# Performance work log

Measured on AMD Instinct MI355X. Metric: run time of the kernel, lower is better.

Reference implementation:

```python
import jax, jax.numpy as jnp
import numpy as np

D_MODEL = 192
D_STATE = 128
D_CONV = 4
EXPAND = 2
D_INNER = EXPAND * D_MODEL            # 384
D_HALF = D_INNER // 2                 # 192 (x and z channel count)
DT_RANK = -(-D_MODEL // 16)           # ceil(192/16) = 12
B, H, W = 8, 32, 32


def serpentine(x):
    # flip every odd row along width: x (b, c, h, w)
    return x.at[:, :, 1::2, :].set(jnp.flip(x[:, :, 1::2, :], axis=3))


def causal_dwconv_silu(x, w):
    # x: (b, d, l), w: (d, k). Left-pad -> causal depthwise conv, then silu.
    k = w.shape[1]
    L = x.shape[-1]
    xp = jnp.pad(x, ((0, 0), (0, 0), (k - 1, 0)))
    y = jnp.zeros_like(x)
    for i in range(k):  # k=4, tiny fixed loop
        y = y + w[:, i][None, :, None] * xp[:, :, i:i + L]
    return jax.nn.silu(y)


def selective_scan(u, delta, A, Bm, Cm, Dp):
    # u, delta: (b, d, l); Bm, Cm: (b, n, l); A: (d, n); Dp: (d,)
    b, d, L = u.shape
    n = A.shape[1]

    def step(h, xs):
        u_t, dt_t, B_t, C_t = xs  # (b,d), (b,d), (b,n), (b,n)
        dA = jnp.exp(dt_t[:, :, None] * A)                      # (b,d,n)
        h = dA * h + (dt_t * u_t)[:, :, None] * B_t[:, None, :]
        y = jnp.einsum('bdn,bn->bd', h, C_t)
        return h, y

    xs = (jnp.moveaxis(u, 2, 0), jnp.moveaxis(delta, 2, 0),
          jnp.moveaxis(Bm, 2, 0), jnp.moveaxis(Cm, 2, 0))
    h0 = jnp.zeros((b, d, n), u.dtype)
    _, ys = jax.lax.scan(step, h0, xs)                          # (l, b, d)
    return jnp.moveaxis(ys, 0, 2).reshape(b, d, L) + Dp[None, :, None] * u


def setup_inputs() -> dict:
    key = jax.random.key(0)
    ks = jax.random.split(key, 8)
    hidden_states = jax.random.normal(ks[0], (B, D_MODEL, H, W), jnp.float32)
    W_in = jax.random.normal(ks[1], (D_INNER, D_MODEL), jnp.float32) * 0.02
    conv_w_x = jax.random.normal(ks[2], (D_HALF, D_CONV), jnp.float32) * 0.2
    conv_w_z = jax.random.normal(ks[3], (D_HALF, D_CONV), jnp.float32) * 0.2
    W_xproj = jax.random.normal(ks[4], (DT_RANK + 2 * D_STATE, D_HALF), jnp.float32) * 0.02
    dt_std = DT_RANK ** (-0.5)
    W_dt = jax.random.uniform(ks[5], (D_HALF, DT_RANK), jnp.float32, -dt_std, dt_std)
    # inv-softplus init of dt bias, as in the module
    dt = jnp.exp(jax.random.uniform(ks[6], (D_HALF,), jnp.float32)
                 * (np.log(0.1) - np.log(0.001)) + np.log(0.001))
    dt = jnp.clip(dt, 1e-4, None)
    b_dt = dt + jnp.log(-jnp.expm1(-dt))
    A_log = jnp.log(jnp.broadcast_to(jnp.arange(1, D_STATE + 1, dtype=jnp.float32),
                                     (D_HALF, D_STATE)))
    D_param = jnp.ones((D_HALF,), jnp.float32)
    W_out = jax.random.normal(ks[7], (D_MODEL, D_INNER), jnp.float32) * 0.02
    return {"hidden_states": hidden_states, "W_in": W_in, "conv_w_x": conv_w_x,
            "conv_w_z": conv_w_z, "W_xproj": W_xproj, "W_dt": W_dt, "b_dt": b_dt,
            "A_log": A_log, "D_param": D_param, "W_out": W_out}


def reference(hidden_states, W_in, conv_w_x, conv_w_z, W_xproj, W_dt, b_dt,
              A_log, D_param, W_out):
    b, c, h, w = hidden_states.shape
    L = h * w
    hs = serpentine(hidden_states)
    hs = hs.reshape(b, c, L).transpose(0, 2, 1)                 # (b, l, c)
    xz = hs @ W_in.T                                            # (b, l, 2d)
    xz = xz.transpose(0, 2, 1)                                  # (b, 2d, l)
    x, z = xz[:, :D_HALF], xz[:, D_HALF:]
    A = -jnp.exp(A_log.astype(jnp.float32))                     # (d, n)
    x = causal_dwconv_silu(x, conv_w_x)
    z = causal_dwconv_silu(z, conv_w_z)
    x_dbl = x.transpose(0, 2, 1) @ W_xproj.T                    # (b, l, r+2n)
    dt = x_dbl[..., :DT_RANK]
    Bm = x_dbl[..., DT_RANK:DT_RANK + D_STATE].transpose(0, 2, 1)  # (b, n, l)
    Cm = x_dbl[..., DT_RANK + D_STATE:].transpose(0, 2, 1)         # (b, n, l)
    dt = (dt @ W_dt.T + b_dt).transpose(0, 2, 1)                # (b, d, l), bias once
    # module passes delta_bias=dt_proj.bias again with delta_softplus=True
    delta = jax.nn.softplus(dt + b_dt[None, :, None])           # bias twice, faithful
    y = selective_scan(x, delta, A, Bm, Cm, D_param.astype(jnp.float32))
    y = jnp.concatenate([y, z], axis=1)                         # (b, 2d, l)
    out = y.transpose(0, 2, 1) @ W_out.T                        # (b, l, c)
    out = out.transpose(0, 2, 1).reshape(b, c, h, w)
    return serpentine(out)
```

## Files before the change

### kernel.cpp

```cpp
#include <hip/hip_runtime.h>
#include <math.h>

#define NB  8
#define DM  192
#define DH  192
#define DI  384
#define DS  128
#define DTR 12
#define XR  268
#define L   1024
#define NC  16
#define CL  64
#define NWX 320
#define LOG2E 1.44269504f

__device__ __forceinline__ void wave_lds_sync() {
  __builtin_amdgcn_wave_barrier();
  asm volatile("s_waitcnt lgkmcnt(0)" ::: "memory");
  __builtin_amdgcn_sched_barrier(0);
}

__global__ void k_wt_all(const float* __restrict__ Win,
                         const float* __restrict__ Wx,
                         const float* __restrict__ Wout,
                         float* __restrict__ wt_in,
                         float* __restrict__ wt_x,
                         float* __restrict__ wt_out) {
  const int j = blockIdx.x * 256 + threadIdx.x;
  const int k = blockIdx.y;
  const int z = blockIdx.z;
  if (z == 0) {
    if (k < 192 && j < 384) wt_in[(size_t)k * 384 + j] = Win[(size_t)j * 192 + k];
  } else if (z == 1) {
    if (k < 192 && j < NWX) wt_x[(size_t)k * NWX + j] = (j < XR) ? Wx[(size_t)j * 192 + k] : 0.f;
  } else {
    if (k < 384 && j < 192) wt_out[(size_t)k * 192 + j] = Wout[(size_t)j * 384 + k];
  }
}

template<int K, int N, int NW, int SERP_IN, int OMODE, int DODT>
__global__ __launch_bounds__(256) void k_gemm(const float* __restrict__ A,
                                              const float* __restrict__ Wt,
                                              float* __restrict__ Out,
                                              const float* __restrict__ Wdt,
                                              const float* __restrict__ bdt,
                                              float* __restrict__ dlt) {
  __shared__ __align__(16) float At2[48][64][4];
  __shared__ float xdl[DODT ? 64 * 13 : 1];
  const int lane = threadIdx.x & 63;
  const int wv   = threadIdx.x >> 6;
  const int l    = blockIdx.x * 64 + lane;
  const int n0   = __builtin_amdgcn_readfirstlane(blockIdx.y * 32 + wv * 8);
  const int b    = blockIdx.z;
  int lg = l;
  if (SERP_IN || OMODE == 2) {
    int h = l >> 5, w = l & 31;
    lg = h * 32 + ((h & 1) ? (31 - w) : w);
  }
  const float* Ab = A + (size_t)b * K * L + (SERP_IN ? lg : l);
  float acc[8];
#pragma unroll
  for (int i = 0; i < 8; ++i) acc[i] = 0.f;

  for (int k0 = 0; k0 < K; k0 += 192) {
    if (k0) __syncthreads();
#pragma unroll
    for (int i = 0; i < 48; ++i) {
      const int kr = wv * 48 + i;
      At2[kr >> 2][lane][kr & 3] = Ab[(size_t)(k0 + kr) * L];
    }
    __syncthreads();
#pragma unroll 8
    for (int kk4 = 0; kk4 < 48; ++kk4) {
      float4 a4 = *(const float4*)&At2[kk4][lane][0];
      float av[4] = {a4.x, a4.y, a4.z, a4.w};
#pragma unroll
      for (int j = 0; j < 4; ++j) {
        const float* wr = Wt + (size_t)(k0 + kk4 * 4 + j) * NW + n0;
        float a = av[j];
#pragma unroll
        for (int i = 0; i < 8; ++i) acc[i] = fmaf(wr[i], a, acc[i]);
      }
    }
  }

  if (OMODE == 0) {
    float* o = Out + ((size_t)b * N + n0) * L + l;
#pragma unroll
    for (int i = 0; i < 8; ++i) o[(size_t)i * L] = acc[i];
  } else if (OMODE == 1) {
    float* o = Out + ((size_t)b * L + l) * XR;
#pragma unroll
    for (int i = 0; i < 8; i += 4) {
      if (n0 + i + 4 <= XR)
        *(float4*)(o + n0 + i) = make_float4(acc[i], acc[i + 1], acc[i + 2], acc[i + 3]);
    }
  } else {
    float* o = Out + ((size_t)b * N + n0) * L + lg;
#pragma unroll
    for (int i = 0; i < 8; ++i) o[(size_t)i * L] = acc[i];
  }

  if constexpr (DODT) {
    if (blockIdx.y == 0) {
      if (wv == 0) {
#pragma unroll
        for (int i = 0; i < 8; ++i) xdl[lane * 13 + i] = acc[i];
      } else if (wv == 1) {
#pragma unroll
        for (int i = 0; i < 4; ++i) xdl[lane * 13 + 8 + i] = acc[i];
      }
      __syncthreads();
      float x[12];
#pragma unroll
      for (int r = 0; r < 12; ++r) x[r] = xdl[lane * 13 + r];
      const int dlo = wv * 48;
      for (int d = dlo; d < dlo + 48; ++d) {
        const float* wd = Wdt + d * DTR;
        float s = 2.f * bdt[d];
#pragma unroll
        for (int r = 0; r < DTR; ++r) s = fmaf(wd[r], x[r], s);
        float v = (s > 20.f) ? s : __logf(1.f + __expf(s));
        dlt[((size_t)b * DH + d) * L + l] = v;
      }
    }
  }
}

__global__ void k_conv_silu(const float* __restrict__ xz,
                            const float* __restrict__ cwx,
                            const float* __restrict__ cwz,
                            float* __restrict__ u,
                            float* __restrict__ ycat) {
  int idx = blockIdx.x * blockDim.x + threadIdx.x;
  const int per = NB * DH * (L / 4);
  int part = idx / per;
  int rem  = idx - part * per;
  int l4 = (rem & (L / 4 - 1)) * 4;
  int bd = rem >> 8;
  int d  = bd % DH;
  int b  = bd / DH;
  const float* cw = (part ? cwz : cwx) + d * 4;
  float w0 = cw[0], w1 = cw[1], w2 = cw[2], w3 = cw[3];
  const float* src = xz + ((size_t)b * DI + (part ? DH + d : d)) * L;
  float4 cur = *(const float4*)(src + l4);
  float pm3 = 0.f, pm2 = 0.f, pm1 = 0.f;
  if (l4 >= 4) {
    float4 p = *(const float4*)(src + l4 - 4);
    pm3 = p.y; pm2 = p.z; pm1 = p.w;
  }
  float s0 = fmaf(w3, cur.x, fmaf(w2, pm1,   fmaf(w1, pm2,   w0 * pm3)));
  float s1 = fmaf(w3, cur.y, fmaf(w2, cur.x, fmaf(w1, pm1,   w0 * pm2)));
  float s2 = fmaf(w3, cur.z, fmaf(w2, cur.y, fmaf(w1, cur.x, w0 * pm1)));
  float s3 = fmaf(w3, cur.w, fmaf(w2, cur.z, fmaf(w1, cur.y, w0 * cur.x)));
  float4 y;
  y.x = s0 / (1.f + __expf(-s0));
  y.y = s1 / (1.f + __expf(-s1));
  y.z = s2 / (1.f + __expf(-s2));
  y.w = s3 / (1.f + __expf(-s3));
  float* dst = part ? (ycat + ((size_t)b * DI + DH + d) * L + l4)
                    : (u + (size_t)bd * L + l4);
  *(float4*)dst = y;
}

__global__ void __launch_bounds__(256) k_scan1(const float* __restrict__ xdbl,
                                               const float* __restrict__ delta,
                                               const float* __restrict__ u,
                                               const float* __restrict__ Alog,
                                               float* __restrict__ hpart,
                                               float* __restrict__ apart) {
  __shared__ __align__(16) float dd[4][64][8];
  const int lane = threadIdx.x & 63;
  const int wv   = threadIdx.x >> 6;
  const int d0   = blockIdx.x * 8 + wv * 2;
  const int c = blockIdx.y, b = blockIdx.z;
  const int bd0 = b * DH + d0, bd1 = bd0 + 1;
  const float a00 = -__expf(Alog[(size_t)d0 * DS + 2 * lane]) * LOG2E;
  const float a10 = -__expf(Alog[(size_t)(d0 + 1) * DS + 2 * lane]) * LOG2E;
  const float* xrow  = xdbl + ((size_t)b * L + c * CL) * XR + DTR + 2 * lane;
  const float* drow0 = delta + (size_t)bd0 * L + c * CL;
  const float* drow1 = delta + (size_t)bd1 * L + c * CL;
  const float* urow0 = u + (size_t)bd0 * L + c * CL;
  const float* urow1 = u + (size_t)bd1 * L + c * CL;
  float dt0 = drow0[lane], u0 = urow0[lane];
  float dt1 = drow1[lane], u1 = urow1[lane];
  *(float4*)&dd[wv][lane][0] =
      make_float4(dt0, dt0 * u0, __builtin_amdgcn_exp2f(-dt0 * LOG2E), 0.f);
  *(float4*)&dd[wv][lane][4] =
      make_float4(dt1, dt1 * u1, __builtin_amdgcn_exp2f(-dt1 * LOG2E), 0.f);
  float s0 = dt0, s1 = dt1;
#pragma unroll
  for (int m = 1; m < 64; m <<= 1) {
    s0 += __shfl_xor(s0, m, 64);
    s1 += __shfl_xor(s1, m, 64);
  }
  wave_lds_sync();
  float h00 = 0.f, h01 = 0.f, h10 = 0.f, h11 = 0.f;
#pragma unroll 8
  for (int t = 0; t < CL; ++t) {
    float4 v0 = *(const float4*)&dd[wv][t][0];
    float4 v1 = *(const float4*)&dd[wv][t][4];
    float2 Bv = *(const float2*)(xrow + (size_t)t * XR);
    float e00 = __builtin_amdgcn_exp2f(v0.x * a00);
    float e01 = e00 * v0.z;
    float e10 = __builtin_amdgcn_exp2f(v1.x * a10);
    float e11 = e10 * v1.z;
    h00 = fmaf(e00, h00, v0.y * Bv.x);
    h01 = fmaf(e01, h01, v0.y * Bv.y);
    h10 = fmaf(e10, h10, v1.y * Bv.x);
    h11 = fmaf(e11, h11, v1.y * Bv.y);
  }
  float ap00 = __builtin_amdgcn_exp2f(s0 * a00);
  float ap01 = ap00 * __builtin_amdgcn_exp2f(-s0 * LOG2E);
  float ap10 = __builtin_amdgcn_exp2f(s1 * a10);
  float ap11 = ap10 * __builtin_amdgcn_exp2f(-s1 * LOG2E);
  *(float2*)(hpart + ((size_t)bd0 * NC + c) * 128 + 2 * lane) = make_float2(h00, h01);
  *(float2*)(hpart + ((size_t)bd1 * NC + c) * 128 + 2 * lane) = make_float2(h10, h11);
  *(float2*)(apart + ((size_t)bd0 * NC + c) * 128 + 2 * lane) = make_float2(ap00, ap01);
  *(float2*)(apart + ((size_t)bd1 * NC + c) * 128 + 2 * lane) = make_float2(ap10, ap11);
}

__global__ void __launch_bounds__(64) k_scan2(float* __restrict__ hpart,
                                              const float* __restrict__ apart) {
  const int bd   = blockIdx.x;
  const int lane = threadIdx.x;
  float H1 = 0.f, H2 = 0.f;
  size_t base = (size_t)bd * (NC * 128) + lane;
  for (int c = 0; c < NC; ++c) {
    size_t o = base + c * 128;
    float hp1 = hpart[o], hp2 = hpart[o + 64];
    float ap1 = apart[o], ap2 = apart[o + 64];
    hpart[o] = H1; hpart[o + 64] = H2;
    H1 = fmaf(ap1, H1, hp1);
    H2 = fmaf(ap2, H2, hp2);
  }
}

__global__ void __launch_bounds__(256) k_scan3(const float* __restrict__ xdbl,
                                               const float* __restrict__ delta,
                                               const float* __restrict__ u,
                                               const float* __restrict__ Alog,
                                               const float* __restrict__ Dp,
                                               const float* __restrict__ hin,
                                               float* __restrict__ ycat) {
  __shared__ __align__(16) float dd[4][64][8];
  __shared__ __align__(16) float pbuf[4][2][8][68];
  const int lane = threadIdx.x & 63;
  const int wv   = threadIdx.x >> 6;
  const int d0   = blockIdx.x * 8 + wv * 2;
  const int c = blockIdx.y, b = blockIdx.z;
  const int bd0 = b * DH + d0, bd1 = bd0 + 1;
  const float a00 = -__expf(Alog[(size_t)d0 * DS + 2 * lane]) * LOG2E;
  const float a10 = -__expf(Alog[(size_t)(d0 + 1) * DS + 2 * lane]) * LOG2E;
  const float* xrow  = xdbl + ((size_t)b * L + c * CL) * XR + DTR + 2 * lane;
  const float* drow0 = delta + (size_t)bd0 * L + c * CL;
  const float* drow1 = delta + (size_t)bd1 * L + c * CL;
  const float* urow0 = u + (size_t)bd0 * L + c * CL;
  const float* urow1 = u + (size_t)bd1 * L + c * CL;
  {
    float dt0 = drow0[lane], u0 = urow0[lane];
    float dt1 = drow1[lane], u1 = urow1[lane];
    *(float4*)&dd[wv][lane][0] =
        make_float4(dt0, dt0 * u0, __builtin_amdgcn_exp2f(-dt0 * LOG2E), 0.f);
    *(float4*)&dd[wv][lane][4] =
        make_float4(dt1, dt1 * u1, __builtin_amdgcn_exp2f(-dt1 * LOG2E), 0.f);
  }
  wave_lds_sync();
  const float* hp0 = hin + ((size_t)bd0 * NC + c) * 128 + 2 * lane;
  const float* hp1 = hin + ((size_t)bd1 * NC + c) * 128 + 2 * lane;
  float2 h0 = *(const float2*)hp0;
  float2 h1 = *(const float2*)hp1;
  const int ch = lane >> 5, pp = (lane >> 3) & 3, tl = lane & 7;
  float* yrow_my = ycat + ((size_t)b * DI + d0 + ch) * L + c * CL;
  const float* urow_my = ch ? urow1 : urow0;
  const float Dd_my = Dp[d0 + ch];

  float2 Br[8], Cr[8];
#pragma unroll
  for (int i = 0; i < 8; ++i) {
    Br[i] = *(const float2*)(xrow + (size_t)i * XR);
    Cr[i] = *(const float2*)(xrow + (size_t)i * XR + DS);
  }

  for (int t8 = 0; t8 < 8; ++t8) {
#pragma unroll
    for (int i = 0; i < 8; ++i) {
      const int t = t8 * 8 + i;
      float4 v0 = *(const float4*)&dd[wv][t][0];
      float4 v1 = *(const float4*)&dd[wv][t][4];
      float e00 = __builtin_amdgcn_exp2f(v0.x * a00);
      float e01 = e00 * v0.z;
      float e10 = __builtin_amdgcn_exp2f(v1.x * a10);
      float e11 = e10 * v1.z;
      h0.x = fmaf(e00, h0.x, v0.y * Br[i].x);
      h0.y = fmaf(e01, h0.y, v0.y * Br[i].y);
      h1.x = fmaf(e10, h1.x, v1.y * Br[i].x);
      h1.y = fmaf(e11, h1.y, v1.y * Br[i].y);
      pbuf[wv][0][i][lane] = fmaf(h0.y, Cr[i].y, h0.x * Cr[i].x);
      pbuf[wv][1][i][lane] = fmaf(h1.y, Cr[i].y, h1.x * Cr[i].x);
    }
    if (t8 < 7) {
#pragma unroll
      for (int i = 0; i < 8; ++i) {
        const int t = (t8 + 1) * 8 + i;
        Br[i] = *(const float2*)(xrow + (size_t)t * XR);
        Cr[i] = *(const float2*)(xrow + (size_t)t * XR + DS);
      }
    }
    wave_lds_sync();
    const float* pr = &pbuf[wv][ch][tl][pp * 16];
    float4 v0 = *(const float4*)(pr);
    float4 v1 = *(const float4*)(pr + 4);
    float4 v2 = *(const float4*)(pr + 8);
    float4 v3 = *(const float4*)(pr + 12);
    float s = (((v0.x + v0.y) + (v0.z + v0.w)) + ((v1.x + v1.y) + (v1.z + v1.w)))
            + (((v2.x + v2.y) + (v2.z + v2.w)) + ((v3.x + v3.y) + (v3.z + v3.w)));
    s += __shfl_xor(s, 8, 64);
    s += __shfl_xor(s, 16, 64);
    if (pp == 0) {
      const int t = t8 * 8 + tl;
      yrow_my[t] = fmaf(Dd_my, urow_my[t], s);
    }
    __builtin_amdgcn_wave_barrier();
  }
}

__global__ void __launch_bounds__(64) k_scan(const float* __restrict__ xdbl,
                                             const float* __restrict__ delta,
                                             const float* __restrict__ u,
                                             const float* __restrict__ Alog,
                                             const float* __restrict__ Dp,
                                             float* __restrict__ ycat) {
  const int bd   = blockIdx.x;
  const int b    = bd / DH;
  const int d    = bd % DH;
  const int lane = threadIdx.x;
  const float a1 = -__expf(Alog[d * DS + lane]);
  const float a2 = -__expf(Alog[d * DS + 64 + lane]);
  const float* xrow = xdbl + (size_t)b * L * XR;
  const float* drow = delta + (size_t)bd * L;
  const float* urow = u + (size_t)bd * L;
  const float Dd = Dp[d];
  float* yrow = ycat + ((size_t)b * DI + d) * L;
  float h1 = 0.f, h2 = 0.f;
  for (int t = 0; t < L; ++t) {
    const float* xd = xrow + (size_t)t * XR;
    float Bv1 = xd[DTR + lane];
    float Bv2 = xd[DTR + 64 + lane];
    float Cv1 = xd[DTR + DS + lane];
    float Cv2 = xd[DTR + DS + 64 + lane];
    float dt = drow[t];
    float ut = urow[t];
    float du = dt * ut;
    h1 = fmaf(__expf(dt * a1), h1, du * Bv1);
    h2 = fmaf(__expf(dt * a2), h2, du * Bv2);
    float p = fmaf(h2, Cv2, h1 * Cv1);
#pragma unroll
    for (int m = 32; m; m >>= 1) p += __shfl_xor(p, m, 64);
    if (lane == 0) yrow[t] = fmaf(Dd, ut, p);
  }
}

extern "C" void kernel_launch(void* const* d_in, const int* in_sizes, int n_in,
                              void* d_out, int out_size, void* d_ws, size_t ws_size,
                              hipStream_t stream) {
  const float* hid  = (const float*)d_in[0];
  const float* Win  = (const float*)d_in[1];
  const float* cwx  = (const float*)d_in[2];
  const float* cwz  = (const float*)d_in[3];
  const float* Wx   = (const float*)d_in[4];
  const float* Wdt  = (const float*)d_in[5];
  const float* bdt  = (const float*)d_in[6];
  const float* Alog = (const float*)d_in[7];
  const float* Dp   = (const float*)d_in[8];
  const float* Wout = (const float*)d_in[9];
  float* out = (float*)d_out;

  float* ws    = (float*)d_ws;
  float* xz    = ws;
  float* u     = xz   + (size_t)NB * DI * L;
  float* ycat  = u    + (size_t)NB * DH * L;
  float* xdbl  = ycat + (size_t)NB * DI * L;
  float* delta = xdbl + (size_t)NB * L * XR;
  float* apart = delta + (size_t)NB * DH * L;
  float* wt_in = apart + (size_t)NB * DH * NC * 128;
  float* wt_x  = wt_in + (size_t)192 * 384;
  float* wt_out= wt_x  + (size_t)192 * NWX;
  float* hpart = xz;

  const size_t need = ((size_t)NB * DI * L * 2 + (size_t)NB * DH * L * 2 +
                       (size_t)NB * L * XR + (size_t)NB * DH * NC * 128 +
                       (size_t)192 * 384 + (size_t)192 * NWX + (size_t)384 * 192) * 4;

  k_wt_all<<<dim3(2, 384, 3), dim3(256), 0, stream>>>(Win, Wx, Wout, wt_in, wt_x, wt_out);

  k_gemm<192, 384, 384, 1, 0, 0><<<dim3(16, 12, NB), dim3(256), 0, stream>>>(
      hid, wt_in, xz, nullptr, nullptr, nullptr);
  k_conv_silu<<<dim3(2 * NB * DH * (L / 4) / 256), dim3(256), 0, stream>>>(xz, cwx, cwz, u, ycat);
  k_gemm<192, XR, NWX, 0, 1, 1><<<dim3(16, 10, NB), dim3(256), 0, stream>>>(
      u, wt_x, xdbl, Wdt, bdt, delta);

  if (ws_size >= need) {
    k_scan1<<<dim3(DH / 8, NC, NB), dim3(256), 0, stream>>>(xdbl, delta, u, Alog, hpart, apart);
    k_scan2<<<dim3(NB * DH), dim3(64), 0, stream>>>(hpart, apart);
    k_scan3<<<dim3(DH / 8, NC, NB), dim3(256), 0, stream>>>(xdbl, delta, u, Alog, Dp, hpart, ycat);
  } else {
    k_scan<<<dim3(NB * DH), dim3(64), 0, stream>>>(xdbl, delta, u, Alog, Dp, ycat);
  }

  k_gemm<384, 192, 192, 0, 2, 0><<<dim3(16, 6, NB), dim3(256), 0, stream>>>(
      ycat, wt_out, out, nullptr, nullptr, nullptr);
}
```

Baseline: 191.6 us.

## Use split-bf16 MFMA for input projection GEMM

Replaces the fp32 SIMT input-projection GEMM with a matrix-core kernel that splits activations and weights into bf16 hi/lo pairs and accumulates three MFMA products to keep near-fp32 accuracy. Weights are pre-split in the transpose kernel, and activations are packed into LDS with the serpentine gather applied on load. The goal is to move the first GEMM onto the matrix units. The cost is three MFMAs per tile, an extra weight-split pass, and a slight accuracy loss from dropping the lo*lo term.

```diff
diff --git a/kernel.cpp b/kernel.cpp
--- a/kernel.cpp
+++ b/kernel.cpp
@@ -14,10 +14,23 @@
 #define NWX 320
 #define LOG2E 1.44269504f
 
+typedef __attribute__((ext_vector_type(8))) short bf16x8;
+typedef __attribute__((ext_vector_type(4))) float f32x4;
+
 __device__ __forceinline__ void wave_lds_sync() {
   __builtin_amdgcn_wave_barrier();
   asm volatile("s_waitcnt lgkmcnt(0)" ::: "memory");
   __builtin_amdgcn_sched_barrier(0);
+}
+
+__device__ __forceinline__ uint32_t pack_bf16x2(float x) {
+  uint32_t u = __float_as_uint(x);
+  uint32_t hi = (u + 0x7fffu + ((u >> 16) & 1u)) >> 16;
+  float hf = __uint_as_float(hi << 16);
+  float lo = x - hf;
+  uint32_t ul = __float_as_uint(lo);
+  uint32_t lo16 = (ul + 0x7fffu + ((ul >> 16) & 1u)) >> 16;
+  return (hi << 16) | (lo16 & 0xffffu);
 }
 
 __global__ void k_wt_all(const float* __restrict__ Win,
@@ -25,7 +38,9 @@
                          const float* __restrict__ Wout,
                          float* __restrict__ wt_in,
                          float* __restrict__ wt_x,
-                         float* __restrict__ wt_out) {
+                         float* __restrict__ wt_out,
+                         ushort* __restrict__ wtn_hi,
+                         ushort* __restrict__ wtn_lo) {
   const int j = blockIdx.x * 256 + threadIdx.x;
   const int k = blockIdx.y;
   const int z = blockIdx.z;
@@ -33,9 +48,78 @@
     if (k < 192 && j < 384) wt_in[(size_t)k * 384 + j] = Win[(size_t)j * 192 + k];
   } else if (z == 1) {
     if (k < 192 && j < NWX) wt_x[(size_t)k * NWX + j] = (j < XR) ? Wx[(size_t)j * 192 + k] : 0.f;
+  } else if (z == 2) {
+    if (k < 384 && j < 192) wt_out[(size_t)k * 192 + j] = Wout[(size_t)j * 384 + k];
   } else {
-    if (k < 384 && j < 192) wt_out[(size_t)k * 192 + j] = Wout[(size_t)j * 384 + k];
-  }
+    const int flat = k * 512 + j;
+    if (j < 512 && flat < 384 * 192) {
+      uint32_t p = pack_bf16x2(Win[flat]);
+      wtn_hi[flat] = (ushort)(p >> 16);
+      wtn_lo[flat] = (ushort)(p & 0xffffu);
+    }
+  }
+}
+
+__global__ __launch_bounds__(256) void k_gemm_in_mfma(
+    const float* __restrict__ A,
+    const ushort* __restrict__ Whi,
+    const ushort* __restrict__ Wlo,
+    float* __restrict__ Out) {
+  __shared__ uint32_t Ap[64][196];
+  const int tid  = threadIdx.x;
+  const int lane = tid & 63;
+  const int wv   = tid >> 6;
+  const int lt = blockIdx.x, nt = blockIdx.y, b = blockIdx.z;
+  const int l = lt * 64 + lane;
+  const int h = l >> 5, w = l & 31;
+  const int lg = h * 32 + ((h & 1) ? (31 - w) : w);
+  const float* Ab = A + (size_t)b * DM * L + lg;
+
+#pragma unroll
+  for (int i = 0; i < 48; ++i) {
+    const int kr = wv * 48 + i;
+    Ap[lane][kr] = pack_bf16x2(Ab[(size_t)kr * L]);
+  }
+  __syncthreads();
+
+  const int ln15 = lane & 15, lq = lane >> 4;
+  f32x4 acc[4];
+#pragma unroll
+  for (int t = 0; t < 4; ++t) acc[t] = (f32x4){0.f, 0.f, 0.f, 0.f};
+
+  const uint32_t* brow = &Ap[wv * 16 + ln15][0];
+#pragma unroll
+  for (int ks = 0; ks < 6; ++ks) {
+    const uint32_t* bp = brow + ks * 32 + lq * 8;
+    uint32_t p0 = bp[0], p1 = bp[1], p2 = bp[2], p3 = bp[3];
+    uint32_t p4 = bp[4], p5 = bp[5], p6 = bp[6], p7 = bp[7];
+    bf16x8 bh, bl;
+    bh[0] = (short)(p0 >> 16); bl[0] = (short)(p0 & 0xffffu);
+    bh[1] = (short)(p1 >> 16); bl[1] = (short)(p1 & 0xffffu);
+    bh[2] = (short)(p2 >> 16); bl[2] = (short)(p2 & 0xffffu);
+    bh[3] = (short)(p3 >> 16); bl[3] = (short)(p3 & 0xffffu);
+    bh[4] = (short)(p4 >> 16); bl[4] = (short)(p4 & 0xffffu);
+    bh[5] = (short)(p5 >> 16); bl[5] = (short)(p5 & 0xffffu);
+    bh[6] = (short)(p6 >> 16); bl[6] = (short)(p6 & 0xffffu);
+    bh[7] = (short)(p7 >> 16); bl[7] = (short)(p7 & 0xffffu);
+#pragma unroll
+    for (int t = 0; t < 4; ++t) {
+      const int n = nt * 64 + t * 16 + ln15;
+      const size_t wo = (size_t)n * DM + ks * 32 + lq * 8;
+      bf16x8 ah = *(const bf16x8*)(Whi + wo);
+      bf16x8 al = *(const bf16x8*)(Wlo + wo);
+      acc[t] = __builtin_amdgcn_mfma_f32_16x16x32_bf16(ah, bh, acc[t], 0, 0, 0);
+      acc[t] = __builtin_amdgcn_mfma_f32_16x16x32_bf16(ah, bl, acc[t], 0, 0, 0);
+      acc[t] = __builtin_amdgcn_mfma_f32_16x16x32_bf16(al, bh, acc[t], 0, 0, 0);
+    }
+  }
+
+  float* ob = Out + ((size_t)b * DI + nt * 64) * L + lt * 64 + wv * 16 + ln15;
+#pragma unroll
+  for (int t = 0; t < 4; ++t)
+#pragma unroll
+    for (int r = 0; r < 4; ++r)
+      ob[(size_t)(t * 16 + lq * 4 + r) * L] = acc[t][r];
 }
 
 template<int K, int N, int NW, int SERP_IN, int OMODE, int DODT>
@@ -386,28 +470,37 @@
   float* wt_in = apart + (size_t)NB * DH * NC * 128;
   float* wt_x  = wt_in + (size_t)192 * 384;
   float* wt_out= wt_x  + (size_t)192 * NWX;
+  ushort* wtn_hi = (ushort*)(wt_out + (size_t)384 * 192);
+  ushort* wtn_lo = wtn_hi + (size_t)384 * 192;
   float* hpart = xz;
 
   const size_t need = ((size_t)NB * DI * L * 2 + (size_t)NB * DH * L * 2 +
                        (size_t)NB * L * XR + (size_t)NB * DH * NC * 128 +
-                       (size_t)192 * 384 + (size_t)192 * NWX + (size_t)384 * 192) * 4;
-
-  k_wt_all<<<dim3(2, 384, 3), dim3(256), 0, stream>>>(Win, Wx, Wout, wt_in, wt_x, wt_out);
-
-  k_gemm<192, 384, 384, 1, 0, 0><<<dim3(16, 12, NB), dim3(256), 0, stream>>>(
-      hid, wt_in, xz, nullptr, nullptr, nullptr);
-  k_conv_silu<<<dim3(2 * NB * DH * (L / 4) / 256), dim3(256), 0, stream>>>(xz, cwx, cwz, u, ycat);
-  k_gemm<192, XR, NWX, 0, 1, 1><<<dim3(16, 10, NB), dim3(256), 0, stream>>>(
-      u, wt_x, xdbl, Wdt, bdt, delta);
+                       (size_t)192 * 384 + (size_t)192 * NWX + (size_t)384 * 192 +
+                       (size_t)384 * 192) * 4;
 
   if (ws_size >= need) {
+    k_wt_all<<<dim3(2, 384, 4), dim3(256), 0, stream>>>(
+        Win, Wx, Wout, wt_in, wt_x, wt_out, wtn_hi, wtn_lo);
+    k_gemm_in_mfma<<<dim3(16, 6, NB), dim3(256), 0, stream>>>(hid, wtn_hi, wtn_lo, xz);
+    k_conv_silu<<<dim3(2 * NB * DH * (L / 4) / 256), dim3(256), 0, stream>>>(xz, cwx, cwz, u, ycat);
+    k_gemm<192, XR, NWX, 0, 1, 1><<<dim3(16, 10, NB), dim3(256), 0, stream>>>(
+        u, wt_x, xdbl, Wdt, bdt, delta);
     k_scan1<<<dim3(DH / 8, NC, NB), dim3(256), 0, stream>>>(xdbl, delta, u, Alog, hpart, apart);
     k_scan2<<<dim3(NB * DH), dim3(64), 0, stream>>>(hpart, apart);
     k_scan3<<<dim3(DH / 8, NC, NB), dim3(256), 0, stream>>>(xdbl, delta, u, Alog, Dp, hpart, ycat);
+    k_gemm<384, 192, 192, 0, 2, 0><<<dim3(16, 6, NB), dim3(256), 0, stream>>>(
+        ycat, wt_out, out, nullptr, nullptr, nullptr);
   } else {
+    k_wt_all<<<dim3(2, 384, 3), dim3(256), 0, stream>>>(
+        Win, Wx, Wout, wt_in, wt_x, wt_out, nullptr, nullptr);
+    k_gemm<192, 384, 384, 1, 0, 0><<<dim3(16, 12, NB), dim3(256), 0, stream>>>(
+        hid, wt_in, xz, nullptr, nullptr, nullptr);
+    k_conv_silu<<<dim3(2 * NB * DH * (L / 4) / 256), dim3(256), 0, stream>>>(xz, cwx, cwz, u, ycat);
+    k_gemm<192, XR, NWX, 0, 1, 1><<<dim3(16, 10, NB), dim3(256), 0, stream>>>(
+        u, wt_x, xdbl, Wdt, bdt, delta);
     k_scan<<<dim3(NB * DH), dim3(64), 0, stream>>>(xdbl, delta, u, Alog, Dp, ycat);
-  }
-
-  k_gemm<384, 192, 192, 0, 2, 0><<<dim3(16, 6, NB), dim3(256), 0, stream>>>(
-      ycat, wt_out, out, nullptr, nullptr, nullptr);
-}
+    k_gemm<384, 192, 192, 0, 2, 0><<<dim3(16, 6, NB), dim3(256), 0, stream>>>(
+        ycat, wt_out, out, nullptr, nullptr, nullptr);
+  }
+}
```

Result: no change. 187.9 us (-1.9%).
